# Kernel tuning notes

Hardware: AMD Instinct MI355X
Metric: run time of the kernel (lower is better)

Reference implementation:

```python
import jax, jax.numpy as jnp
import numpy as np

V = 50257; E = 1024; H = 1024; L = 256; NL = 2; D = 10


def setup_inputs() -> dict:
    key = jax.random.key(0)
    ks = jax.random.split(key, 16)
    n = lambda k, s: jax.random.normal(k, s, dtype=jnp.float32)
    return {
        "input_tok": jax.random.randint(ks[0], (1, 1), 0, V),
        "h0": n(ks[1], (NL, 1, H)),
        "c0": n(ks[2], (NL, 1, H)),
        "h_s": n(ks[3], (L, 1, H)),
        "h_t_tilde": n(ks[4], (1, 1, H)),
        "emb": n(ks[5], (V, E)) * 0.02,
        "Wp": n(ks[6], (H, H)) * (H ** -0.5),
        "wdot": n(ks[7], (1, H)) * (H ** -0.5),
        "Wbil": n(ks[8], (1, H, H)) * (H ** -0.5),
        "Wcomb": n(ks[9], (H, 2 * H)) * ((2 * H) ** -0.5),
        "bcomb": jnp.zeros((H,), jnp.float32),
        "Wih0": n(ks[10], (4 * H, E + H)) * ((E + H) ** -0.5),
        "Whh0": n(ks[11], (4 * H, H)) * (H ** -0.5),
        "bih0": jnp.zeros((4 * H,), jnp.float32),
        "bhh0": jnp.zeros((4 * H,), jnp.float32),
        "Wih1": n(ks[12], (4 * H, H)) * (H ** -0.5),
        "Whh1": n(ks[13], (4 * H, H)) * (H ** -0.5),
        "bih1": jnp.zeros((4 * H,), jnp.float32),
        "bhh1": jnp.zeros((4 * H,), jnp.float32),
        "Wout": n(ks[14], (V, H)) * (H ** -0.5),
        "bout": jnp.zeros((V,), jnp.float32),
    }


def _lstm_cell(x, h, c, Wih, Whh, bih, bhh):
    # torch LSTM gate order: i, f, g, o
    g = x @ Wih.T + bih + h @ Whh.T + bhh
    i, f, gg, o = jnp.split(g, 4, axis=-1)
    c2 = jax.nn.sigmoid(f) * c + jax.nn.sigmoid(i) * jnp.tanh(gg)
    h2 = jax.nn.sigmoid(o) * jnp.tanh(c2)
    return h2, c2


def reference(input_tok, h0, c0, h_s, h_t_tilde, emb, Wp, wdot, Wbil, Wcomb, bcomb,
              Wih0, Whh0, bih0, bhh0, Wih1, Whh1, bih1, bhh1, Wout, bout):
    embedding = emb[input_tok]                                  # [1,1,E]
    x = jnp.concatenate((embedding, h_t_tilde), axis=-1)[0]     # [1,E+H]
    h1, c1 = _lstm_cell(x, h0[0], c0[0], Wih0, Whh0, bih0, bhh0)
    h2, c2 = _lstm_cell(h1, h0[1], c0[1], Wih1, Whh1, bih1, bhh1)
    h_new = jnp.stack((h1, h2)); c_new = jnp.stack((c1, c2))
    h_t = h2                                                    # [1,H]
    Ls = h_s.shape[0]
    p_t = Ls * jax.nn.sigmoid(jnp.tanh(h_t @ Wp.T) @ wdot.T).squeeze()  # scalar
    s = jnp.round(p_t).astype(jnp.int32)
    idx = jnp.arange(Ls)
    lo = jnp.maximum(s - D, 0); hi = jnp.minimum(s + D, Ls - 1)
    mask = (idx >= lo) & (idx <= hi)                            # [L] local window
    # bilinear score h_t^T W h_s over all positions; mask outside window
    score = jnp.einsum('bh,ohk,lbk->lbo', h_t, Wbil, h_s)       # [L,1,1]
    neg = jnp.finfo(score.dtype).min
    a = jax.nn.softmax(jnp.where(mask[:, None, None], score, neg), axis=0)
    # NOTE: original uses exp(+d^2/(D/2)^2) (no minus sign); replicated faithfully.
    expo = jnp.where(mask, ((idx.astype(jnp.float32) - p_t) ** 2) / ((D / 2) ** 2), 0.0)
    a_t = a * jnp.exp(expo)[:, None, None]                      # [L,1,1]
    win = (hi - lo + 1).astype(jnp.float32)
    context = jnp.sum(a_t * h_s, axis=0, keepdims=True) / win   # [1,1,H] (mean over window)
    cat = jnp.concatenate((context, h_t[None]), axis=-1)        # [1,1,2H]
    h_t_tilde_new = jnp.tanh(cat @ Wcomb.T + bcomb)             # [1,1,H]
    y = jax.nn.log_softmax(h_t_tilde_new @ Wout.T + bout, axis=-1)  # [1,1,V]
    return (y, h_new, c_new, h_t_tilde_new, a_t, p_t)
```

## Files before the change

kernel.cpp:

```cpp
#include <hip/hip_runtime.h>
#include <math.h>

#define V 50257
#define E 1024
#define HH 1024
#define LL 256

#define O_H  (V)
#define O_C  (V + 2*HH)
#define O_HT (V + 4*HH)
#define O_A  (V + 5*HH)
#define O_P  (V + 5*HH + LL)

#define W_T    0
#define W_V    1024
#define W_SC   2048
#define W_CTX  2304
#define W_Z    4096
#define W_BM   54400
#define W_BS   55424
#define W_LOGZ 56448

#define NB_LOGITS 786

__device__ __forceinline__ float sigmoidf_(float x) { return 1.f / (1.f + expf(-x)); }

__device__ __forceinline__ float block_sum(float v, float* red) {
    int lane = threadIdx.x & 63, wv = threadIdx.x >> 6;
#pragma unroll
    for (int o = 32; o > 0; o >>= 1) v += __shfl_down(v, o, 64);
    if (lane == 0) red[wv] = v;
    __syncthreads();
    return red[0] + red[1] + red[2] + red[3];
}

__global__ void k_lstm(const float* __restrict__ Wih, const float* __restrict__ Whh,
                       const float* __restrict__ bih, const float* __restrict__ bhh,
                       const float* __restrict__ xa_base, const int* __restrict__ tok,
                       const float* __restrict__ xb, int na, int nb,
                       const float* __restrict__ hprev, const float* __restrict__ cprev,
                       float* __restrict__ hout, float* __restrict__ cout) {
    const int u = blockIdx.x;
    const int K = na + nb;
    const float* xa = tok ? (xa_base + (size_t)tok[0] * na) : xa_base;
    const float* r0 = Wih + (size_t)u * K;
    const float* r1 = Wih + (size_t)(u + HH) * K;
    const float* r2 = Wih + (size_t)(u + 2*HH) * K;
    const float* r3 = Wih + (size_t)(u + 3*HH) * K;
    float a0 = 0, a1 = 0, a2 = 0, a3 = 0;
    for (int j = threadIdx.x; j < K; j += 256) {
        float xv = (j < na) ? xa[j] : xb[j - na];
        a0 += r0[j] * xv; a1 += r1[j] * xv; a2 += r2[j] * xv; a3 += r3[j] * xv;
    }
    const float* s0 = Whh + (size_t)u * HH;
    const float* s1 = Whh + (size_t)(u + HH) * HH;
    const float* s2 = Whh + (size_t)(u + 2*HH) * HH;
    const float* s3 = Whh + (size_t)(u + 3*HH) * HH;
    for (int j = threadIdx.x; j < HH; j += 256) {
        float hv = hprev[j];
        a0 += s0[j] * hv; a1 += s1[j] * hv; a2 += s2[j] * hv; a3 += s3[j] * hv;
    }
    int lane = threadIdx.x & 63, wv = threadIdx.x >> 6;
#pragma unroll
    for (int o = 32; o > 0; o >>= 1) {
        a0 += __shfl_down(a0, o, 64);
        a1 += __shfl_down(a1, o, 64);
        a2 += __shfl_down(a2, o, 64);
        a3 += __shfl_down(a3, o, 64);
    }
    __shared__ float sm[4][4];
    if (lane == 0) { sm[wv][0] = a0; sm[wv][1] = a1; sm[wv][2] = a2; sm[wv][3] = a3; }
    __syncthreads();
    if (threadIdx.x == 0) {
        float gi = sm[0][0]+sm[1][0]+sm[2][0]+sm[3][0] + bih[u]        + bhh[u];
        float gf = sm[0][1]+sm[1][1]+sm[2][1]+sm[3][1] + bih[u+HH]     + bhh[u+HH];
        float gg = sm[0][2]+sm[1][2]+sm[2][2]+sm[3][2] + bih[u+2*HH]   + bhh[u+2*HH];
        float go = sm[0][3]+sm[1][3]+sm[2][3]+sm[3][3] + bih[u+3*HH]   + bhh[u+3*HH];
        float c = sigmoidf_(gf) * cprev[u] + sigmoidf_(gi) * tanhf(gg);
        hout[u] = sigmoidf_(go) * tanhf(c);
        cout[u] = c;
    }
}

__global__ void k_ptv(const float* __restrict__ Wp, const float* __restrict__ Wbil,
                      const float* __restrict__ h2, float* __restrict__ t_out,
                      float* __restrict__ v_out) {
    __shared__ float red[4];
    if (blockIdx.x < HH) {
        int r = blockIdx.x;
        const float* row = Wp + (size_t)r * HH;
        float acc = 0;
        for (int j = threadIdx.x; j < HH; j += 256) acc += row[j] * h2[j];
        float tot = block_sum(acc, red);
        if (threadIdx.x == 0) t_out[r] = tanhf(tot);
    } else {
        int b = blockIdx.x - HH;
        int hc = b >> 2, kc = b & 3;
        int k = kc * 256 + threadIdx.x;
        int h0 = hc * 32;
        float acc = 0;
        for (int h = h0; h < h0 + 32; ++h) acc += h2[h] * Wbil[(size_t)h * HH + k];
        atomicAdd(&v_out[k], acc);
    }
}

__global__ void k_score_p(const float* __restrict__ wdot, const float* __restrict__ t,
                          const float* __restrict__ v, const float* __restrict__ hs,
                          float* __restrict__ score, float* __restrict__ pt) {
    __shared__ float red[4];
    if (blockIdx.x == 0) {
        float acc = 0;
        for (int j = threadIdx.x; j < HH; j += 256) acc += wdot[j] * t[j];
        float tot = block_sum(acc, red);
        if (threadIdx.x == 0) pt[0] = (float)LL * sigmoidf_(tot);
    } else {
        int l = blockIdx.x - 1;
        const float* row = hs + (size_t)l * HH;
        float acc = 0;
        for (int j = threadIdx.x; j < HH; j += 256) acc += row[j] * v[j];
        float tot = block_sum(acc, red);
        if (threadIdx.x == 0) score[l] = tot;
    }
}

__global__ void k_soft(const float* __restrict__ score, const float* __restrict__ pt,
                       float* __restrict__ a_out) {
    int l = threadIdx.x;
    float p = pt[0];
    int si = (int)rintf(p);
    int lo = max(si - 10, 0), hi = min(si + 10, LL - 1);
    bool mask = (l >= lo) && (l <= hi);
    float sc = score[l];
    __shared__ float sm[256];
    sm[l] = mask ? sc : -INFINITY;
    __syncthreads();
    for (int s = 128; s > 0; s >>= 1) { if (l < s) sm[l] = fmaxf(sm[l], sm[l + s]); __syncthreads(); }
    float M = sm[0];
    __syncthreads();
    float e = mask ? expf(sc - M) : 0.f;
    sm[l] = e;
    __syncthreads();
    for (int s = 128; s > 0; s >>= 1) { if (l < s) sm[l] += sm[l + s]; __syncthreads(); }
    float S = sm[0];
    float a = e / S;
    float d = (float)l - p;
    a_out[l] = mask ? a * expf(d * d * 0.04f) : 0.f;
}

__global__ void k_ctx(const float* __restrict__ a_t, const float* __restrict__ hs,
                      float* __restrict__ ctx) {
    int hc = blockIdx.x & 3, lc = blockIdx.x >> 2;
    int h = hc * 256 + threadIdx.x;
    int l0 = lc * 16;
    float acc = 0;
    for (int l = l0; l < l0 + 16; ++l) {
        float a = a_t[l];
        if (a != 0.f) acc += a * hs[(size_t)l * HH + h];
    }
    if (acc != 0.f) atomicAdd(&ctx[h], acc);
}

__global__ void k_comb(const float* __restrict__ Wcomb, const float* __restrict__ bcomb,
                       const float* __restrict__ ctx, const float* __restrict__ h2,
                       const float* __restrict__ pt, float* __restrict__ outv) {
    __shared__ float red[4];
    int u = blockIdx.x;
    float p = pt[0];
    int si = (int)rintf(p);
    int lo = max(si - 10, 0), hi = min(si + 10, LL - 1);
    float inv_win = 1.f / (float)(hi - lo + 1);
    const float* row = Wcomb + (size_t)u * (2 * HH);
    float acc = 0;
    for (int j = threadIdx.x; j < 2 * HH; j += 256) {
        float xv = (j < HH) ? ctx[j] * inv_win : h2[j - HH];
        acc += row[j] * xv;
    }
    float tot = block_sum(acc, red);
    if (threadIdx.x == 0) outv[u] = tanhf(tot + bcomb[u]);
}

__global__ void k_logits(const float* __restrict__ Wout, const float* __restrict__ bout,
                         const float* __restrict__ x, float* __restrict__ z,
                         float* __restrict__ bmax, float* __restrict__ bsum) {
    __shared__ float sx[1024];
    for (int j = threadIdx.x; j < 1024; j += 256) sx[j] = x[j];
    __syncthreads();
    int lane = threadIdx.x & 63, wv = threadIdx.x >> 6;
    int base = blockIdx.x * 64 + wv * 16;
    float m = -INFINITY, s = 0.f;
    for (int t = 0; t < 16; ++t) {
        int r = base + t;
        if (r >= V) break;
        const float* row = Wout + (size_t)r * 1024;
        float acc = 0;
#pragma unroll
        for (int j = 0; j < 16; ++j) acc += row[lane + 64 * j] * sx[lane + 64 * j];
#pragma unroll
        for (int o = 32; o > 0; o >>= 1) acc += __shfl_xor(acc, o, 64);
        float zz = acc + bout[r];
        if (lane == 0) z[r] = zz;
        if (zz > m) { s *= expf(m - zz); m = zz; }
        s += expf(zz - m);
    }
    __shared__ float wm[4], wsv[4];
    if (lane == 0) { wm[wv] = m; wsv[wv] = s; }
    __syncthreads();
    if (threadIdx.x == 0) {
        float M = fmaxf(fmaxf(wm[0], wm[1]), fmaxf(wm[2], wm[3]));
        float S = 0.f;
        if (M != -INFINITY) {
#pragma unroll
            for (int w = 0; w < 4; ++w)
                if (wm[w] != -INFINITY) S += wsv[w] * expf(wm[w] - M);
        }
        bmax[blockIdx.x] = M; bsum[blockIdx.x] = S;
    }
}

__global__ void k_lse(const float* __restrict__ bmax, const float* __restrict__ bsum,
                      int n, float* __restrict__ logZ) {
    int tid = threadIdx.x;
    float m = -INFINITY, s = 0.f;
    for (int i = tid; i < n; i += 256) {
        float m2 = bmax[i], s2 = bsum[i];
        float M = fmaxf(m, m2);
        if (M != -INFINITY) s = s * expf(m - M) + s2 * expf(m2 - M);
        m = M;
    }
    int lane = tid & 63, wv = tid >> 6;
#pragma unroll
    for (int o = 32; o > 0; o >>= 1) {
        float m2 = __shfl_down(m, o, 64), s2 = __shfl_down(s, o, 64);
        float M = fmaxf(m, m2);
        if (M != -INFINITY) s = s * expf(m - M) + s2 * expf(m2 - M);
        else s = 0.f;
        m = M;
    }
    __shared__ float wm[4], wsv[4];
    if (lane == 0) { wm[wv] = m; wsv[wv] = s; }
    __syncthreads();
    if (tid == 0) {
        float M = -INFINITY, S = 0.f;
#pragma unroll
        for (int w = 0; w < 4; ++w) {
            float M2 = fmaxf(M, wm[w]);
            if (M2 != -INFINITY) S = S * expf(M - M2) + wsv[w] * expf(wm[w] - M2);
            M = M2;
        }
        logZ[0] = M + logf(S);
    }
}

__global__ void k_sub(const float* __restrict__ z, const float* __restrict__ logZ,
                      float* __restrict__ y) {
    int i = blockIdx.x * 256 + threadIdx.x;
    if (i < V) y[i] = z[i] - logZ[0];
}

extern "C" void kernel_launch(void* const* d_in, const int* in_sizes, int n_in,
                              void* d_out, int out_size, void* d_ws, size_t ws_size,
                              hipStream_t stream) {
    const int*   tok   = (const int*)  d_in[0];
    const float* h0    = (const float*)d_in[1];
    const float* c0    = (const float*)d_in[2];
    const float* hs    = (const float*)d_in[3];
    const float* htt   = (const float*)d_in[4];
    const float* emb   = (const float*)d_in[5];
    const float* Wp    = (const float*)d_in[6];
    const float* wdot  = (const float*)d_in[7];
    const float* Wbil  = (const float*)d_in[8];
    const float* Wcomb = (const float*)d_in[9];
    const float* bcomb = (const float*)d_in[10];
    const float* Wih0  = (const float*)d_in[11];
    const float* Whh0  = (const float*)d_in[12];
    const float* bih0  = (const float*)d_in[13];
    const float* bhh0  = (const float*)d_in[14];
    const float* Wih1  = (const float*)d_in[15];
    const float* Whh1  = (const float*)d_in[16];
    const float* bih1  = (const float*)d_in[17];
    const float* bhh1  = (const float*)d_in[18];
    const float* Wout  = (const float*)d_in[19];
    const float* bout  = (const float*)d_in[20];

    float* out = (float*)d_out;
    float* ws  = (float*)d_ws;

    float* h1o  = out + O_H;
    float* h2o  = out + O_H + HH;
    float* c1o  = out + O_C;
    float* c2o  = out + O_C + HH;
    float* htto = out + O_HT;
    float* ato  = out + O_A;
    float* pto  = out + O_P;

    hipMemsetAsync(ws, 0, 3328 * sizeof(float), stream);

    hipLaunchKernelGGL(k_lstm, dim3(1024), dim3(256), 0, stream,
                       Wih0, Whh0, bih0, bhh0, emb, tok, htt, 1024, 1024,
                       h0, c0, h1o, c1o);
    hipLaunchKernelGGL(k_lstm, dim3(1024), dim3(256), 0, stream,
                       Wih1, Whh1, bih1, bhh1, h1o, (const int*)nullptr, h1o, 1024, 0,
                       h0 + HH, c0 + HH, h2o, c2o);
    hipLaunchKernelGGL(k_ptv, dim3(1024 + 128), dim3(256), 0, stream,
                       Wp, Wbil, h2o, ws + W_T, ws + W_V);
    hipLaunchKernelGGL(k_score_p, dim3(257), dim3(256), 0, stream,
                       wdot, ws + W_T, ws + W_V, hs, ws + W_SC, pto);
    hipLaunchKernelGGL(k_soft, dim3(1), dim3(256), 0, stream,
                       ws + W_SC, pto, ato);
    hipLaunchKernelGGL(k_ctx, dim3(64), dim3(256), 0, stream,
                       ato, hs, ws + W_CTX);
    hipLaunchKernelGGL(k_comb, dim3(1024), dim3(256), 0, stream,
                       Wcomb, bcomb, ws + W_CTX, h2o, pto, htto);
    hipLaunchKernelGGL(k_logits, dim3(NB_LOGITS), dim3(256), 0, stream,
                       Wout, bout, htto, ws + W_Z, ws + W_BM, ws + W_BS);
    hipLaunchKernelGGL(k_lse, dim3(1), dim3(256), 0, stream,
                       ws + W_BM, ws + W_BS, NB_LOGITS, ws + W_LOGZ);
    hipLaunchKernelGGL(k_sub, dim3((V + 255) / 256), dim3(256), 0, stream,
                       ws + W_Z, ws + W_LOGZ, out);
}
```

Baseline: 101.6 us.

## Vectorize GEMV loads with float4 and fuse small kernels to cut launches

Every matrix-vector kernel now loads weights and vectors as float4. The memset is dropped: the first LSTM launch zeros the bilinear accumulator. Softmax and context are merged into one 5-block kernel that writes context directly without atomics. The log-sum-exp reduction is folded into the subtraction kernel. These changes cut launch count and widen memory transactions. In exchange, every block of the final kernel now redundantly recomputes the 786-entry reduction, and the float4 paths assume the sizes are divisible by 4 and the rows are aligned.

```diff
diff --git a/kernel.cpp b/kernel.cpp
--- a/kernel.cpp
+++ b/kernel.cpp
@@ -19,11 +19,13 @@
 #define W_Z    4096
 #define W_BM   54400
 #define W_BS   55424
-#define W_LOGZ 56448
 
 #define NB_LOGITS 786
 
 __device__ __forceinline__ float sigmoidf_(float x) { return 1.f / (1.f + expf(-x)); }
+__device__ __forceinline__ float dot4(float4 a, float4 b) {
+    return a.x * b.x + a.y * b.y + a.z * b.z + a.w * b.w;
+}
 
 __device__ __forceinline__ float block_sum(float v, float* red) {
     int lane = threadIdx.x & 63, wv = threadIdx.x >> 6;
@@ -39,26 +41,35 @@
                        const float* __restrict__ xa_base, const int* __restrict__ tok,
                        const float* __restrict__ xb, int na, int nb,
                        const float* __restrict__ hprev, const float* __restrict__ cprev,
-                       float* __restrict__ hout, float* __restrict__ cout) {
+                       float* __restrict__ hout, float* __restrict__ cout,
+                       float* __restrict__ zero_buf) {
     const int u = blockIdx.x;
     const int K = na + nb;
+    const int K4 = K >> 2, na4 = na >> 2;
+    if (zero_buf && threadIdx.x == 0) zero_buf[u] = 0.f;
     const float* xa = tok ? (xa_base + (size_t)tok[0] * na) : xa_base;
-    const float* r0 = Wih + (size_t)u * K;
-    const float* r1 = Wih + (size_t)(u + HH) * K;
-    const float* r2 = Wih + (size_t)(u + 2*HH) * K;
-    const float* r3 = Wih + (size_t)(u + 3*HH) * K;
+    const float4* xa4 = (const float4*)xa;
+    const float4* xb4 = (const float4*)xb;
+    const float4* r0 = (const float4*)(Wih + (size_t)u * K);
+    const float4* r1 = (const float4*)(Wih + (size_t)(u + HH) * K);
+    const float4* r2 = (const float4*)(Wih + (size_t)(u + 2*HH) * K);
+    const float4* r3 = (const float4*)(Wih + (size_t)(u + 3*HH) * K);
     float a0 = 0, a1 = 0, a2 = 0, a3 = 0;
-    for (int j = threadIdx.x; j < K; j += 256) {
-        float xv = (j < na) ? xa[j] : xb[j - na];
-        a0 += r0[j] * xv; a1 += r1[j] * xv; a2 += r2[j] * xv; a3 += r3[j] * xv;
-    }
-    const float* s0 = Whh + (size_t)u * HH;
-    const float* s1 = Whh + (size_t)(u + HH) * HH;
-    const float* s2 = Whh + (size_t)(u + 2*HH) * HH;
-    const float* s3 = Whh + (size_t)(u + 3*HH) * HH;
-    for (int j = threadIdx.x; j < HH; j += 256) {
-        float hv = hprev[j];
-        a0 += s0[j] * hv; a1 += s1[j] * hv; a2 += s2[j] * hv; a3 += s3[j] * hv;
+    for (int j = threadIdx.x; j < K4; j += 256) {
+        float4 xv = (j < na4) ? xa4[j] : xb4[j - na4];
+        a0 += dot4(r0[j], xv); a1 += dot4(r1[j], xv);
+        a2 += dot4(r2[j], xv); a3 += dot4(r3[j], xv);
+    }
+    const float4* s0 = (const float4*)(Whh + (size_t)u * HH);
+    const float4* s1 = (const float4*)(Whh + (size_t)(u + HH) * HH);
+    const float4* s2 = (const float4*)(Whh + (size_t)(u + 2*HH) * HH);
+    const float4* s3 = (const float4*)(Whh + (size_t)(u + 3*HH) * HH);
+    const float4* hp4 = (const float4*)hprev;
+    {
+        int j = threadIdx.x;
+        float4 hv = hp4[j];
+        a0 += dot4(s0[j], hv); a1 += dot4(s1[j], hv);
+        a2 += dot4(s2[j], hv); a3 += dot4(s3[j], hv);
     }
     int lane = threadIdx.x & 63, wv = threadIdx.x >> 6;
 #pragma unroll
@@ -88,19 +99,27 @@
     __shared__ float red[4];
     if (blockIdx.x < HH) {
         int r = blockIdx.x;
-        const float* row = Wp + (size_t)r * HH;
-        float acc = 0;
-        for (int j = threadIdx.x; j < HH; j += 256) acc += row[j] * h2[j];
+        const float4* row = (const float4*)(Wp + (size_t)r * HH);
+        const float4* h24 = (const float4*)h2;
+        float acc = dot4(row[threadIdx.x], h24[threadIdx.x]);
         float tot = block_sum(acc, red);
         if (threadIdx.x == 0) t_out[r] = tanhf(tot);
     } else {
         int b = blockIdx.x - HH;
-        int hc = b >> 2, kc = b & 3;
-        int k = kc * 256 + threadIdx.x;
-        int h0 = hc * 32;
-        float acc = 0;
-        for (int h = h0; h < h0 + 32; ++h) acc += h2[h] * Wbil[(size_t)h * HH + k];
-        atomicAdd(&v_out[k], acc);
+        int h0 = b * 32;
+        int k4 = threadIdx.x;
+        const float4* W4 = (const float4*)Wbil;
+        float4 acc = make_float4(0.f, 0.f, 0.f, 0.f);
+        for (int h = h0; h < h0 + 32; ++h) {
+            float hv = h2[h];
+            float4 w = W4[(size_t)h * 256 + k4];
+            acc.x += hv * w.x; acc.y += hv * w.y;
+            acc.z += hv * w.z; acc.w += hv * w.w;
+        }
+        atomicAdd(&v_out[k4 * 4 + 0], acc.x);
+        atomicAdd(&v_out[k4 * 4 + 1], acc.y);
+        atomicAdd(&v_out[k4 * 4 + 2], acc.z);
+        atomicAdd(&v_out[k4 * 4 + 3], acc.w);
     }
 }
 
@@ -109,22 +128,24 @@
                           float* __restrict__ score, float* __restrict__ pt) {
     __shared__ float red[4];
     if (blockIdx.x == 0) {
-        float acc = 0;
-        for (int j = threadIdx.x; j < HH; j += 256) acc += wdot[j] * t[j];
+        const float4* w4 = (const float4*)wdot;
+        const float4* t4 = (const float4*)t;
+        float acc = dot4(w4[threadIdx.x], t4[threadIdx.x]);
         float tot = block_sum(acc, red);
         if (threadIdx.x == 0) pt[0] = (float)LL * sigmoidf_(tot);
     } else {
         int l = blockIdx.x - 1;
-        const float* row = hs + (size_t)l * HH;
-        float acc = 0;
-        for (int j = threadIdx.x; j < HH; j += 256) acc += row[j] * v[j];
+        const float4* row = (const float4*)(hs + (size_t)l * HH);
+        const float4* v4  = (const float4*)v;
+        float acc = dot4(row[threadIdx.x], v4[threadIdx.x]);
         float tot = block_sum(acc, red);
         if (threadIdx.x == 0) score[l] = tot;
     }
 }
 
-__global__ void k_soft(const float* __restrict__ score, const float* __restrict__ pt,
-                       float* __restrict__ a_out) {
+__global__ void k_ctx(const float* __restrict__ score, const float* __restrict__ pt,
+                      const float* __restrict__ hs, float* __restrict__ ctx,
+                      float* __restrict__ a_out) {
     int l = threadIdx.x;
     float p = pt[0];
     int si = (int)rintf(p);
@@ -132,6 +153,7 @@
     bool mask = (l >= lo) && (l <= hi);
     float sc = score[l];
     __shared__ float sm[256];
+    __shared__ float sa[256];
     sm[l] = mask ? sc : -INFINITY;
     __syncthreads();
     for (int s = 128; s > 0; s >>= 1) { if (l < s) sm[l] = fmaxf(sm[l], sm[l + s]); __syncthreads(); }
@@ -142,22 +164,18 @@
     __syncthreads();
     for (int s = 128; s > 0; s >>= 1) { if (l < s) sm[l] += sm[l + s]; __syncthreads(); }
     float S = sm[0];
-    float a = e / S;
     float d = (float)l - p;
-    a_out[l] = mask ? a * expf(d * d * 0.04f) : 0.f;
-}
-
-__global__ void k_ctx(const float* __restrict__ a_t, const float* __restrict__ hs,
-                      float* __restrict__ ctx) {
-    int hc = blockIdx.x & 3, lc = blockIdx.x >> 2;
-    int h = hc * 256 + threadIdx.x;
-    int l0 = lc * 16;
-    float acc = 0;
-    for (int l = l0; l < l0 + 16; ++l) {
-        float a = a_t[l];
-        if (a != 0.f) acc += a * hs[(size_t)l * HH + h];
-    }
-    if (acc != 0.f) atomicAdd(&ctx[h], acc);
+    sa[l] = mask ? (e / S) * expf(d * d * 0.04f) : 0.f;
+    __syncthreads();
+    if (blockIdx.x == 4) {
+        a_out[l] = sa[l];
+    } else {
+        int h = blockIdx.x * 256 + l;
+        float acc = 0.f;
+        for (int ll = lo; ll <= hi; ++ll)
+            acc += sa[ll] * hs[(size_t)ll * HH + h];
+        ctx[h] = acc;
+    }
 }
 
 __global__ void k_comb(const float* __restrict__ Wcomb, const float* __restrict__ bcomb,
@@ -169,11 +187,20 @@
     int si = (int)rintf(p);
     int lo = max(si - 10, 0), hi = min(si + 10, LL - 1);
     float inv_win = 1.f / (float)(hi - lo + 1);
-    const float* row = Wcomb + (size_t)u * (2 * HH);
+    const float4* row  = (const float4*)(Wcomb + (size_t)u * (2 * HH));
+    const float4* ctx4 = (const float4*)ctx;
+    const float4* h24  = (const float4*)h2;
     float acc = 0;
-    for (int j = threadIdx.x; j < 2 * HH; j += 256) {
-        float xv = (j < HH) ? ctx[j] * inv_win : h2[j - HH];
-        acc += row[j] * xv;
+#pragma unroll
+    for (int j = threadIdx.x; j < 512; j += 256) {
+        float4 xv;
+        if (j < 256) {
+            xv = ctx4[j];
+            xv.x *= inv_win; xv.y *= inv_win; xv.z *= inv_win; xv.w *= inv_win;
+        } else {
+            xv = h24[j - 256];
+        }
+        acc += dot4(row[j], xv);
     }
     float tot = block_sum(acc, red);
     if (threadIdx.x == 0) outv[u] = tanhf(tot + bcomb[u]);
@@ -182,8 +209,8 @@
 __global__ void k_logits(const float* __restrict__ Wout, const float* __restrict__ bout,
                          const float* __restrict__ x, float* __restrict__ z,
                          float* __restrict__ bmax, float* __restrict__ bsum) {
-    __shared__ float sx[1024];
-    for (int j = threadIdx.x; j < 1024; j += 256) sx[j] = x[j];
+    __shared__ float4 sx[256];
+    sx[threadIdx.x] = ((const float4*)x)[threadIdx.x];
     __syncthreads();
     int lane = threadIdx.x & 63, wv = threadIdx.x >> 6;
     int base = blockIdx.x * 64 + wv * 16;
@@ -191,10 +218,11 @@
     for (int t = 0; t < 16; ++t) {
         int r = base + t;
         if (r >= V) break;
-        const float* row = Wout + (size_t)r * 1024;
+        const float4* row = (const float4*)(Wout + (size_t)r * 1024);
         float acc = 0;
 #pragma unroll
-        for (int j = 0; j < 16; ++j) acc += row[lane + 64 * j] * sx[lane + 64 * j];
+        for (int j = 0; j < 4; ++j)
+            acc += dot4(row[lane + 64 * j], sx[lane + 64 * j]);
 #pragma unroll
         for (int o = 32; o > 0; o >>= 1) acc += __shfl_xor(acc, o, 64);
         float zz = acc + bout[r];
@@ -217,8 +245,8 @@
     }
 }
 
-__global__ void k_lse(const float* __restrict__ bmax, const float* __restrict__ bsum,
-                      int n, float* __restrict__ logZ) {
+__global__ void k_sub(const float* __restrict__ z, const float* __restrict__ bmax,
+                      const float* __restrict__ bsum, int n, float* __restrict__ y) {
     int tid = threadIdx.x;
     float m = -INFINITY, s = 0.f;
     for (int i = tid; i < n; i += 256) {
@@ -237,6 +265,7 @@
         m = M;
     }
     __shared__ float wm[4], wsv[4];
+    __shared__ float lzs;
     if (lane == 0) { wm[wv] = m; wsv[wv] = s; }
     __syncthreads();
     if (tid == 0) {
@@ -247,14 +276,12 @@
             if (M2 != -INFINITY) S = S * expf(M - M2) + wsv[w] * expf(wm[w] - M2);
             M = M2;
         }
-        logZ[0] = M + logf(S);
-    }
-}
-
-__global__ void k_sub(const float* __restrict__ z, const float* __restrict__ logZ,
-                      float* __restrict__ y) {
-    int i = blockIdx.x * 256 + threadIdx.x;
-    if (i < V) y[i] = z[i] - logZ[0];
+        lzs = M + logf(S);
+    }
+    __syncthreads();
+    float lz = lzs;
+    int i = blockIdx.x * 256 + tid;
+    if (i < V) y[i] = z[i] - lz;
 }
 
 extern "C" void kernel_launch(void* const* d_in, const int* in_sizes, int n_in,
@@ -293,28 +320,22 @@
     float* ato  = out + O_A;
     float* pto  = out + O_P;
 
-    hipMemsetAsync(ws, 0, 3328 * sizeof(float), stream);
-
     hipLaunchKernelGGL(k_lstm, dim3(1024), dim3(256), 0, stream,
                        Wih0, Whh0, bih0, bhh0, emb, tok, htt, 1024, 1024,
-                       h0, c0, h1o, c1o);
+                       h0, c0, h1o, c1o, ws + W_V);
     hipLaunchKernelGGL(k_lstm, dim3(1024), dim3(256), 0, stream,
                        Wih1, Whh1, bih1, bhh1, h1o, (const int*)nullptr, h1o, 1024, 0,
-                       h0 + HH, c0 + HH, h2o, c2o);
-    hipLaunchKernelGGL(k_ptv, dim3(1024 + 128), dim3(256), 0, stream,
+                       h0 + HH, c0 + HH, h2o, c2o, (float*)nullptr);
+    hipLaunchKernelGGL(k_ptv, dim3(1024 + 32), dim3(256), 0, stream,
                        Wp, Wbil, h2o, ws + W_T, ws + W_V);
     hipLaunchKernelGGL(k_score_p, dim3(257), dim3(256), 0, stream,
                        wdot, ws + W_T, ws + W_V, hs, ws + W_SC, pto);
-    hipLaunchKernelGGL(k_soft, dim3(1), dim3(256), 0, stream,
-                       ws + W_SC, pto, ato);
-    hipLaunchKernelGGL(k_ctx, dim3(64), dim3(256), 0, stream,
-                       ato, hs, ws + W_CTX);
+    hipLaunchKernelGGL(k_ctx, dim3(5), dim3(256), 0, stream,
+                       ws + W_SC, pto, hs, ws + W_CTX, ato);
     hipLaunchKernelGGL(k_comb, dim3(1024), dim3(256), 0, stream,
                        Wcomb, bcomb, ws + W_CTX, h2o, pto, htto);
     hipLaunchKernelGGL(k_logits, dim3(NB_LOGITS), dim3(256), 0, stream,
                        Wout, bout, htto, ws + W_Z, ws + W_BM, ws + W_BS);
-    hipLaunchKernelGGL(k_lse, dim3(1), dim3(256), 0, stream,
-                       ws + W_BM, ws + W_BS, NB_LOGITS, ws + W_LOGZ);
     hipLaunchKernelGGL(k_sub, dim3((V + 255) / 256), dim3(256), 0, stream,
-                       ws + W_Z, ws + W_LOGZ, out);
-}
+                       ws + W_Z, ws + W_BM, ws + W_BS, NB_LOGITS, out);
+}
```

Measured after the change: 91.27 us. 10.2% less time.
